# Kernel optimization log

Hardware: AMD Instinct MI355X
Metric: run time of the kernel (lower is better)

## Reference

```python
import jax, jax.numpy as jnp
import numpy as np

NUM_HEADS = 8
CHUNK = 64


def _retention(q, k, v):
    # q, k: (B, H, L, DK); v: (B, H, L, DV). Chunked linear retention with
    # per-head exponential decay gamma_h = 1 - 2^(-5-h) (RetNet convention).
    B, Hn, L, DK = q.shape
    DV = v.shape[-1]
    C = CHUNK
    N = L // C
    dt = q.dtype
    gamma = (1.0 - jnp.exp2(-5.0 - jnp.arange(Hn, dtype=jnp.float32))).astype(dt)  # (H,)
    q = q * (DK ** -0.5)
    idx = jnp.arange(C)
    diff = idx[:, None] - idx[None, :]
    # intra-chunk causal decay mask D[h,i,j] = gamma_h^(i-j) for i>=j else 0
    D = jnp.where(diff >= 0, gamma[:, None, None] ** diff, 0.0).astype(dt)      # (H,C,C)
    decay_q = (gamma[:, None] ** (idx[None, :] + 1)).astype(dt)                 # (H,C)
    decay_k = (gamma[:, None] ** (C - 1 - idx[None, :])).astype(dt)             # (H,C)
    decay_s = (gamma ** C).astype(dt)                                           # (H,)

    def to_chunks(x):
        return jnp.moveaxis(x.reshape(B, Hn, N, C, -1), 2, 0)  # (N,B,H,C,d)

    qs, ks, vs = map(to_chunks, (q, k, v))

    def step(S, x):
        qc, kc, vc = x  # (B,H,C,dk) / (B,H,C,dv)
        attn = jnp.einsum('bhid,bhjd->bhij', qc, kc) * D
        o_intra = jnp.einsum('bhij,bhje->bhie', attn, vc)
        o_inter = jnp.einsum('bhid,bhde->bhie', qc * decay_q[None, :, :, None], S)
        S_new = decay_s[None, :, None, None] * S + jnp.einsum(
            'bhjd,bhje->bhde', kc * decay_k[None, :, :, None], vc)
        return S_new, o_intra + o_inter

    S0 = jnp.zeros((B, Hn, DK, DV), dt)
    _, o = jax.lax.scan(step, S0, (qs, ks, vs))  # (N,B,H,C,DV)
    return jnp.moveaxis(o, 0, 2).reshape(B, Hn, L, DV)


def _xavier(key, fan_in, fan_out, gain=2 ** (-2.5)):
    limit = gain * np.sqrt(6.0 / (fan_in + fan_out))
    return jax.random.uniform(key, (fan_in, fan_out), jnp.float32, -limit, limit)


def setup_inputs() -> dict:
    key = jax.random.key(0)
    k0, k1, k2, k3, k4 = jax.random.split(key, 5)
    B, L, D = 2, 4096, 1024
    return {
        'hidden_states': jax.random.normal(k0, (B, L, D), jnp.float32),
        'rel_pos': jnp.zeros((1,), jnp.float32),  # unused by the module's forward
        'Wq': _xavier(k1, D, D),
        'Wk': _xavier(k2, D, D),
        'Wv': _xavier(k3, D, D),
        'Wo': _xavier(k4, D, D),
    }


def reference(hidden_states, rel_pos, Wq, Wk, Wv, Wo):
    B, L, Dm = hidden_states.shape
    Hd = Dm // NUM_HEADS
    q = (hidden_states @ Wq).reshape(B, L, NUM_HEADS, Hd).transpose(0, 2, 1, 3)
    k = (hidden_states @ Wk).reshape(B, L, NUM_HEADS, Hd).transpose(0, 2, 1, 3)
    v = (hidden_states @ Wv).reshape(B, L, NUM_HEADS, Hd).transpose(0, 2, 1, 3)
    o = _retention(q, k, v)  # (B,H,L,Hd)
    o = o.transpose(0, 2, 1, 3).reshape(B, L, Dm)
    return o @ Wo
```

## Files before the change

### kernel.cpp

```cpp
#include <hip/hip_runtime.h>
#include <hip/hip_bf16.h>

typedef __bf16 bf16;
typedef __bf16 bf16x8 __attribute__((ext_vector_type(8)));
typedef float f32x4 __attribute__((ext_vector_type(4)));

#define MFMA16(a, b, c) __builtin_amdgcn_mfma_f32_16x16x32_bf16((a), (b), (c), 0, 0, 0)


__device__ __forceinline__ void g2l16(const bf16* g, bf16* l) {
  __builtin_amdgcn_global_load_lds(
      (const __attribute__((address_space(1))) void*)g,
      (__attribute__((address_space(3))) void*)l, 16, 0, 0);
}

__global__ __launch_bounds__(256) void cvt_bf16(const float* __restrict__ X,
                                                bf16* __restrict__ Y) {
  const size_t i = ((size_t)blockIdx.x * 256 + threadIdx.x) * 8;
  float4 a = *(const float4*)&X[i];
  float4 b = *(const float4*)&X[i + 4];
  union { bf16 h[8]; uint4 u; } p;
  p.h[0] = (bf16)a.x; p.h[1] = (bf16)a.y; p.h[2] = (bf16)a.z; p.h[3] = (bf16)a.w;
  p.h[4] = (bf16)b.x; p.h[5] = (bf16)b.y; p.h[6] = (bf16)b.z; p.h[7] = (bf16)b.w;
  *(uint4*)&Y[i] = p.u;
}

__global__ __launch_bounds__(256) void transpose_w(
    const float* __restrict__ Wq, const float* __restrict__ Wk,
    const float* __restrict__ Wv, const float* __restrict__ Wo,
    bf16* __restrict__ Wt) {
  __shared__ bf16 t[64 * 72];
  const float* src = (blockIdx.z == 0) ? Wq : (blockIdx.z == 1) ? Wk
                     : (blockIdx.z == 2) ? Wv : Wo;
  bf16* dst = Wt + (size_t)blockIdx.z * 1024 * 1024;
  const int k0 = blockIdx.x * 64, n0 = blockIdx.y * 64;
  const int tid = threadIdx.x;
#pragma unroll
  for (int s = 0; s < 4; ++s) {
    int u = tid + s * 256;
    int r = u >> 4, c4 = (u & 15) * 4;
    float4 f = *(const float4*)&src[(size_t)(k0 + r) * 1024 + n0 + c4];
    t[r * 72 + c4 + 0] = (bf16)f.x;
    t[r * 72 + c4 + 1] = (bf16)f.y;
    t[r * 72 + c4 + 2] = (bf16)f.z;
    t[r * 72 + c4 + 3] = (bf16)f.w;
  }
  __syncthreads();
#pragma unroll
  for (int s = 0; s < 2; ++s) {
    int u = tid + s * 256;
    int r = u >> 3, cc = u & 7;
    union { bf16 h[8]; uint4 u4; } pk;
#pragma unroll
    for (int j = 0; j < 8; ++j) pk.h[j] = t[(cc * 8 + j) * 72 + r];
    *(uint4*)&dst[(size_t)(n0 + r) * 1024 + k0 + cc * 8] = pk.u4;
  }
}

template <typename TC, int QKV>
__global__ __launch_bounds__(256) void gemm_lds(
    const bf16* __restrict__ A, const bf16* __restrict__ Bt,
    TC* __restrict__ C, float alpha) {
  __shared__ bf16 lA[128 * 64];
  __shared__ bf16 lB[128 * 64];
  const int m0 = blockIdx.x * 128, n0 = blockIdx.y * 128;
  if (QKV) {
    Bt += (size_t)blockIdx.z * 1024 * 1024;
    C += (size_t)blockIdx.z * 8192 * 1024;
    if (blockIdx.z != 0) alpha = 1.0f;
  }
  const int tid = threadIdx.x;
  const int w = tid >> 6, lane = tid & 63, lr = lane & 15, quad = lane >> 4;
  const int wm = w >> 1, wn = w & 1;

  const int srow = w * 32 + (lane >> 3);
  const int clog = (lane & 7) ^ ((lane >> 3) & 7);
  const bf16* gA = A + (size_t)(m0 + srow) * 1024 + clog * 8;
  const bf16* gB = Bt + (size_t)(n0 + srow) * 1024 + clog * 8;

  f32x4 acc[4][4] = {};

  for (int it = 0; it < 16; ++it) {
    const int k0 = it * 64;
#pragma unroll
    for (int is = 0; is < 4; ++is) {
      g2l16(gA + (size_t)is * 8 * 1024 + k0, &lA[(w * 32 + is * 8) * 64]);
      g2l16(gB + (size_t)is * 8 * 1024 + k0, &lB[(w * 32 + is * 8) * 64]);
    }
    __syncthreads();
#pragma unroll
    for (int kk = 0; kk < 2; ++kk) {
      bf16x8 af[4], bfv[4];
#pragma unroll
      for (int i = 0; i < 4; ++i) {
        const int m = wm * 64 + i * 16 + lr;
        af[i] = *(bf16x8*)&lA[m * 64 + (((kk * 4 + quad) ^ (lr & 7)) * 8)];
      }
#pragma unroll
      for (int j = 0; j < 4; ++j) {
        const int n = wn * 64 + j * 16 + lr;
        bfv[j] = *(bf16x8*)&lB[n * 64 + (((kk * 4 + quad) ^ (lr & 7)) * 8)];
      }
#pragma unroll
      for (int i = 0; i < 4; ++i)
#pragma unroll
        for (int j = 0; j < 4; ++j)
          acc[i][j] = MFMA16(af[i], bfv[j], acc[i][j]);
    }
    __syncthreads();
  }
#pragma unroll
  for (int i = 0; i < 4; ++i) {
#pragma unroll
    for (int j = 0; j < 4; ++j) {
      const int row = m0 + wm * 64 + i * 16 + quad * 4;
      const int col = n0 + wn * 64 + j * 16 + lr;
#pragma unroll
      for (int r = 0; r < 4; ++r)
        C[(size_t)(row + r) * 1024 + col] = (TC)(acc[i][j][r] * alpha);
    }
  }
}

__global__ __launch_bounds__(256) void chunk_kv(
    const bf16* __restrict__ kb, const bf16* __restrict__ vb,
    bf16* __restrict__ Tb) {
  __shared__ bf16 lK[128 * 72];
  __shared__ bf16 lV[128 * 72];
  const int g = blockIdx.x;
  const int bh = g >> 6, n = g & 63, b = bh >> 3, h = bh & 7;
  const float log2g = log2f(1.0f - exp2f(-5.0f - (float)h));
  const int tid = threadIdx.x;
  const size_t rowbase = (size_t)(b * 4096 + n * 64) * 1024 + h * 128;
  const bf16* kc = kb + rowbase;
  const bf16* vc = vb + rowbase;
#pragma unroll
  for (int s = 0; s < 4; ++s) {
    int u = tid + s * 256;
    int c = u >> 4, d0 = (u & 15) * 8;
    union { uint4 u4; bf16 h8[8]; } kv, vv;
    kv.u4 = *(const uint4*)&kc[(size_t)c * 1024 + d0];
    vv.u4 = *(const uint4*)&vc[(size_t)c * 1024 + d0];
    const float dec = exp2f((float)(63 - c) * log2g);
#pragma unroll
    for (int j = 0; j < 8; ++j) {
      lK[(d0 + j) * 72 + c] = (bf16)((float)kv.h8[j] * dec);
      lV[(d0 + j) * 72 + c] = vv.h8[j];
    }
  }
  __syncthreads();
  const int w = tid >> 6, lane = tid & 63, lr = lane & 15, quad = lane >> 4;
  const int wm = w >> 1, wn = w & 1;
  f32x4 acc[4][4] = {};
#pragma unroll
  for (int kk = 0; kk < 2; ++kk) {
    bf16x8 af[4], bv[4];
#pragma unroll
    for (int i = 0; i < 4; ++i)
      af[i] = *(bf16x8*)&lK[(wm * 64 + i * 16 + lr) * 72 + kk * 32 + quad * 8];
#pragma unroll
    for (int j = 0; j < 4; ++j)
      bv[j] = *(bf16x8*)&lV[(wn * 64 + j * 16 + lr) * 72 + kk * 32 + quad * 8];
#pragma unroll
    for (int i = 0; i < 4; ++i)
#pragma unroll
      for (int j = 0; j < 4; ++j)
        acc[i][j] = MFMA16(af[i], bv[j], acc[i][j]);
  }
  bf16* tchunk = Tb + (size_t)g * 16384;
#pragma unroll
  for (int i = 0; i < 4; ++i) {
#pragma unroll
    for (int j = 0; j < 4; ++j) {
      const int dk = wm * 64 + i * 16 + quad * 4;
      const int dv = wn * 64 + j * 16 + lr;
      union { bf16 h4[4]; uint2 u2; } pk;
#pragma unroll
      for (int r = 0; r < 4; ++r) pk.h4[r] = (bf16)acc[i][j][r];
      *(uint2*)&tchunk[(size_t)dv * 128 + dk] = pk.u2;
    }
  }
}

__global__ __launch_bounds__(256) void scan_state(bf16* __restrict__ Tb) {
  const int blk = blockIdx.x;
  const int bh = blk >> 6, seg = blk & 63, h = bh & 7;
  const float gs = exp2f(64.0f * log2f(1.0f - exp2f(-5.0f - (float)h)));
  const size_t base = (size_t)bh * 64 * 16384 + (size_t)seg * 256 + threadIdx.x;
  float S = 0.0f;
#pragma unroll 8
  for (int n = 0; n < 64; ++n) {
    const size_t a = base + (size_t)n * 16384;
    const float t = (float)Tb[a];
    Tb[a] = (bf16)S;
    S = gs * S + t;
  }
}

__global__ __launch_bounds__(256) void chunk_out(
    const bf16* __restrict__ qb, const bf16* __restrict__ kb,
    const bf16* __restrict__ vb, const bf16* __restrict__ Sp,
    bf16* __restrict__ ob) {
  __shared__ bf16 lQ[64 * 136];
  __shared__ bf16 lK[64 * 136];
  __shared__ bf16 lVt[128 * 72];
  __shared__ bf16 lP[64 * 72];
  const int g = blockIdx.x;
  const int bh = g >> 6, n = g & 63, b = bh >> 3, h = bh & 7;
  const float log2g = log2f(1.0f - exp2f(-5.0f - (float)h));
  const int tid = threadIdx.x;
  const size_t rowbase = (size_t)(b * 4096 + n * 64) * 1024 + h * 128;
  const bf16* qc = qb + rowbase;
  const bf16* kc = kb + rowbase;
  const bf16* vc = vb + rowbase;
#pragma unroll
  for (int s = 0; s < 4; ++s) {
    int u = tid + s * 256;
    int c = u >> 4, d0 = (u & 15) * 8;
    *(uint4*)&lQ[c * 136 + d0] = *(const uint4*)&qc[(size_t)c * 1024 + d0];
    *(uint4*)&lK[c * 136 + d0] = *(const uint4*)&kc[(size_t)c * 1024 + d0];
    union { uint4 u4; bf16 h8[8]; } vv;
    vv.u4 = *(const uint4*)&vc[(size_t)c * 1024 + d0];
#pragma unroll
    for (int j = 0; j < 8; ++j) lVt[(d0 + j) * 72 + c] = vv.h8[j];
  }
  __syncthreads();
  const int w = tid >> 6, lane = tid & 63, lr = lane & 15, quad = lane >> 4;

  f32x4 p[4] = {};
#pragma unroll
  for (int kk = 0; kk < 4; ++kk) {
    bf16x8 bfrag = *(bf16x8*)&lK[(w * 16 + lr) * 136 + kk * 32 + quad * 8];
#pragma unroll
    for (int i = 0; i < 4; ++i) {
      bf16x8 afrag = *(bf16x8*)&lQ[(i * 16 + lr) * 136 + kk * 32 + quad * 8];
      p[i] = MFMA16(afrag, bfrag, p[i]);
    }
  }
#pragma unroll
  for (int i = 0; i < 4; ++i) {
#pragma unroll
    for (int r = 0; r < 4; ++r) {
      const int row = i * 16 + quad * 4 + r;
      const int col = w * 16 + lr;
      const int diff = row - col;
      const float val =
          (diff >= 0) ? p[i][r] * exp2f((float)diff * log2g) : 0.0f;
      lP[row * 72 + col] = (bf16)val;
    }
  }
  __syncthreads();

  f32x4 oacc[4][2] = {};
#pragma unroll
  for (int j = 0; j < 2; ++j) {
    const int dvt = w * 32 + j * 16;
#pragma unroll
    for (int kk = 0; kk < 2; ++kk) {
      bf16x8 bfrag = *(bf16x8*)&lVt[(dvt + lr) * 72 + kk * 32 + quad * 8];
#pragma unroll
      for (int i = 0; i < 4; ++i) {
        bf16x8 afrag = *(bf16x8*)&lP[(i * 16 + lr) * 72 + kk * 32 + quad * 8];
        oacc[i][j] = MFMA16(afrag, bfrag, oacc[i][j]);
      }
    }
  }

  const bf16* sp = Sp + (size_t)g * 16384;
#pragma unroll
  for (int kk = 0; kk < 4; ++kk) {
    bf16x8 aN[4];
#pragma unroll
    for (int i = 0; i < 4; ++i) {
      bf16x8 a0 = *(bf16x8*)&lQ[(i * 16 + lr) * 136 + kk * 32 + quad * 8];
      const float dq = exp2f((float)(i * 16 + lr + 1) * log2g);
#pragma unroll
      for (int e = 0; e < 8; ++e) a0[e] = (bf16)((float)a0[e] * dq);
      aN[i] = a0;
    }
#pragma unroll
    for (int j = 0; j < 2; ++j) {
      bf16x8 bfrag =
          *(const bf16x8*)&sp[(size_t)(w * 32 + j * 16 + lr) * 128 + kk * 32 + quad * 8];
#pragma unroll
      for (int i = 0; i < 4; ++i) oacc[i][j] = MFMA16(aN[i], bfrag, oacc[i][j]);
    }
  }

  bf16* oc = ob + rowbase;
#pragma unroll
  for (int i = 0; i < 4; ++i)
#pragma unroll
    for (int j = 0; j < 2; ++j)
#pragma unroll
      for (int r = 0; r < 4; ++r) {
        const int row = i * 16 + quad * 4 + r;
        const int col = w * 32 + j * 16 + lr;
        oc[(size_t)row * 1024 + col] = (bf16)oacc[i][j][r];
      }
}

extern "C" void kernel_launch(void* const* d_in, const int* in_sizes, int n_in,
                              void* d_out, int out_size, void* d_ws,
                              size_t ws_size, hipStream_t stream) {
  const float* X  = (const float*)d_in[0];
  const float* Wq = (const float*)d_in[2];
  const float* Wk = (const float*)d_in[3];
  const float* Wv = (const float*)d_in[4];
  const float* Wo = (const float*)d_in[5];

  char* ws = (char*)d_ws;
  const size_t SZ_QKV = (size_t)8192 * 1024 * sizeof(bf16);
  bf16* qb = (bf16*)(ws);
  bf16* ob = (bf16*)(ws + 3 * SZ_QKV);
  bf16* Tb = (bf16*)(ws + 4 * SZ_QKV);
  bf16* Wt = (bf16*)(ws + 6 * SZ_QKV);
  bf16* Xb = (bf16*)(ws + 6 * SZ_QKV + (size_t)4 * 1024 * 1024 * sizeof(bf16));
  bf16* kb = qb + (size_t)8192 * 1024;
  bf16* vb = kb + (size_t)8192 * 1024;

  cvt_bf16<<<4096, 256, 0, stream>>>(X, Xb);
  transpose_w<<<dim3(16, 16, 4), 256, 0, stream>>>(Wq, Wk, Wv, Wo, Wt);

  const float qscale = 0.08838834764831845f;
  gemm_lds<bf16, 1><<<dim3(64, 8, 3), 256, 0, stream>>>(Xb, Wt, qb, qscale);

  chunk_kv<<<1024, 256, 0, stream>>>(kb, vb, Tb);
  scan_state<<<1024, 256, 0, stream>>>(Tb);
  chunk_out<<<1024, 256, 0, stream>>>(qb, kb, vb, Tb, ob);

  gemm_lds<float, 0><<<dim3(64, 8), 256, 0, stream>>>(
      ob, Wt + (size_t)3 * 1024 * 1024, (float*)d_out, 1.0f);
}
```

Baseline: 230.9 us.

## Merge prep kernels, swizzle transposed LDS tiles, vectorize state scan, precompute decayed Q

Fuses the input conversion and weight transpose into a single launch. Applies an XOR swizzle to the transposed K/V LDS tiles in chunk_kv and chunk_out to reduce bank conflicts on the strided column writes. Rewrites scan_state so each thread handles 8 contiguous elements with 16-byte loads, using 128 blocks instead of 1024. chunk_out now builds a decay-scaled copy of Q in LDS once, instead of rescaling fragments inside the inter-chunk MMA loop, at the cost of extra shared memory.

```diff
diff --git a/kernel.cpp b/kernel.cpp
--- a/kernel.cpp
+++ b/kernel.cpp
@@ -14,27 +14,32 @@
       (__attribute__((address_space(3))) void*)l, 16, 0, 0);
 }
 
-__global__ __launch_bounds__(256) void cvt_bf16(const float* __restrict__ X,
-                                                bf16* __restrict__ Y) {
-  const size_t i = ((size_t)blockIdx.x * 256 + threadIdx.x) * 8;
-  float4 a = *(const float4*)&X[i];
-  float4 b = *(const float4*)&X[i + 4];
-  union { bf16 h[8]; uint4 u; } p;
-  p.h[0] = (bf16)a.x; p.h[1] = (bf16)a.y; p.h[2] = (bf16)a.z; p.h[3] = (bf16)a.w;
-  p.h[4] = (bf16)b.x; p.h[5] = (bf16)b.y; p.h[6] = (bf16)b.z; p.h[7] = (bf16)b.w;
-  *(uint4*)&Y[i] = p.u;
-}
-
-__global__ __launch_bounds__(256) void transpose_w(
-    const float* __restrict__ Wq, const float* __restrict__ Wk,
-    const float* __restrict__ Wv, const float* __restrict__ Wo,
+__device__ __forceinline__ int swz72(int row, int c) {
+  return row * 72 + (c & 7) + ((((c >> 3) ^ (row >> 3)) & 7) << 3);
+}
+
+__global__ __launch_bounds__(256) void prep(
+    const float* __restrict__ X, const float* __restrict__ Wq,
+    const float* __restrict__ Wk, const float* __restrict__ Wv,
+    const float* __restrict__ Wo, bf16* __restrict__ Xb,
     bf16* __restrict__ Wt) {
   __shared__ bf16 t[64 * 72];
-  const float* src = (blockIdx.z == 0) ? Wq : (blockIdx.z == 1) ? Wk
-                     : (blockIdx.z == 2) ? Wv : Wo;
-  bf16* dst = Wt + (size_t)blockIdx.z * 1024 * 1024;
-  const int k0 = blockIdx.x * 64, n0 = blockIdx.y * 64;
   const int tid = threadIdx.x;
+  if (blockIdx.x < 4096) {
+    const size_t i = ((size_t)blockIdx.x * 256 + tid) * 8;
+    float4 a = *(const float4*)&X[i];
+    float4 b = *(const float4*)&X[i + 4];
+    union { bf16 h[8]; uint4 u; } p;
+    p.h[0] = (bf16)a.x; p.h[1] = (bf16)a.y; p.h[2] = (bf16)a.z; p.h[3] = (bf16)a.w;
+    p.h[4] = (bf16)b.x; p.h[5] = (bf16)b.y; p.h[6] = (bf16)b.z; p.h[7] = (bf16)b.w;
+    *(uint4*)&Xb[i] = p.u;
+    return;
+  }
+  const int bid2 = blockIdx.x - 4096;
+  const int bx = bid2 & 15, by = (bid2 >> 4) & 15, bz = bid2 >> 8;
+  const float* src = (bz == 0) ? Wq : (bz == 1) ? Wk : (bz == 2) ? Wv : Wo;
+  bf16* dst = Wt + (size_t)bz * 1024 * 1024;
+  const int k0 = bx * 64, n0 = by * 64;
 #pragma unroll
   for (int s = 0; s < 4; ++s) {
     int u = tid + s * 256;
@@ -144,8 +149,8 @@
     const float dec = exp2f((float)(63 - c) * log2g);
 #pragma unroll
     for (int j = 0; j < 8; ++j) {
-      lK[(d0 + j) * 72 + c] = (bf16)((float)kv.h8[j] * dec);
-      lV[(d0 + j) * 72 + c] = vv.h8[j];
+      lK[swz72(d0 + j, c)] = (bf16)((float)kv.h8[j] * dec);
+      lV[swz72(d0 + j, c)] = vv.h8[j];
     }
   }
   __syncthreads();
@@ -157,10 +162,10 @@
     bf16x8 af[4], bv[4];
 #pragma unroll
     for (int i = 0; i < 4; ++i)
-      af[i] = *(bf16x8*)&lK[(wm * 64 + i * 16 + lr) * 72 + kk * 32 + quad * 8];
+      af[i] = *(bf16x8*)&lK[swz72(wm * 64 + i * 16 + lr, kk * 32 + quad * 8)];
 #pragma unroll
     for (int j = 0; j < 4; ++j)
-      bv[j] = *(bf16x8*)&lV[(wn * 64 + j * 16 + lr) * 72 + kk * 32 + quad * 8];
+      bv[j] = *(bf16x8*)&lV[swz72(wn * 64 + j * 16 + lr, kk * 32 + quad * 8)];
 #pragma unroll
     for (int i = 0; i < 4; ++i)
 #pragma unroll
@@ -184,16 +189,22 @@
 
 __global__ __launch_bounds__(256) void scan_state(bf16* __restrict__ Tb) {
   const int blk = blockIdx.x;
-  const int bh = blk >> 6, seg = blk & 63, h = bh & 7;
+  const int bh = blk >> 3, seg = blk & 7, h = bh & 7;
   const float gs = exp2f(64.0f * log2f(1.0f - exp2f(-5.0f - (float)h)));
-  const size_t base = (size_t)bh * 64 * 16384 + (size_t)seg * 256 + threadIdx.x;
-  float S = 0.0f;
-#pragma unroll 8
+  const size_t base = (size_t)bh * 64 * 16384 + (size_t)seg * 2048 +
+                      (size_t)threadIdx.x * 8;
+  float S[8] = {0.f, 0.f, 0.f, 0.f, 0.f, 0.f, 0.f, 0.f};
+#pragma unroll 4
   for (int n = 0; n < 64; ++n) {
     const size_t a = base + (size_t)n * 16384;
-    const float t = (float)Tb[a];
-    Tb[a] = (bf16)S;
-    S = gs * S + t;
+    union { uint4 u4; bf16 h8[8]; } in, out;
+    in.u4 = *(const uint4*)&Tb[a];
+#pragma unroll
+    for (int e = 0; e < 8; ++e) {
+      out.h8[e] = (bf16)S[e];
+      S[e] = gs * S[e] + (float)in.h8[e];
+    }
+    *(uint4*)&Tb[a] = out.u4;
   }
 }
 
@@ -202,6 +213,7 @@
     const bf16* __restrict__ vb, const bf16* __restrict__ Sp,
     bf16* __restrict__ ob) {
   __shared__ bf16 lQ[64 * 136];
+  __shared__ bf16 lQd[64 * 136];
   __shared__ bf16 lK[64 * 136];
   __shared__ bf16 lVt[128 * 72];
   __shared__ bf16 lP[64 * 72];
@@ -217,12 +229,17 @@
   for (int s = 0; s < 4; ++s) {
     int u = tid + s * 256;
     int c = u >> 4, d0 = (u & 15) * 8;
-    *(uint4*)&lQ[c * 136 + d0] = *(const uint4*)&qc[(size_t)c * 1024 + d0];
+    union { uint4 u4; bf16 h8[8]; } qv, vv, qd;
+    qv.u4 = *(const uint4*)&qc[(size_t)c * 1024 + d0];
+    *(uint4*)&lQ[c * 136 + d0] = qv.u4;
     *(uint4*)&lK[c * 136 + d0] = *(const uint4*)&kc[(size_t)c * 1024 + d0];
-    union { uint4 u4; bf16 h8[8]; } vv;
+    const float dq = exp2f((float)(c + 1) * log2g);
+#pragma unroll
+    for (int j = 0; j < 8; ++j) qd.h8[j] = (bf16)((float)qv.h8[j] * dq);
+    *(uint4*)&lQd[c * 136 + d0] = qd.u4;
     vv.u4 = *(const uint4*)&vc[(size_t)c * 1024 + d0];
 #pragma unroll
-    for (int j = 0; j < 8; ++j) lVt[(d0 + j) * 72 + c] = vv.h8[j];
+    for (int j = 0; j < 8; ++j) lVt[swz72(d0 + j, c)] = vv.h8[j];
   }
   __syncthreads();
   const int w = tid >> 6, lane = tid & 63, lr = lane & 15, quad = lane >> 4;
@@ -257,7 +274,7 @@
     const int dvt = w * 32 + j * 16;
 #pragma unroll
     for (int kk = 0; kk < 2; ++kk) {
-      bf16x8 bfrag = *(bf16x8*)&lVt[(dvt + lr) * 72 + kk * 32 + quad * 8];
+      bf16x8 bfrag = *(bf16x8*)&lVt[swz72(dvt + lr, kk * 32 + quad * 8)];
 #pragma unroll
       for (int i = 0; i < 4; ++i) {
         bf16x8 afrag = *(bf16x8*)&lP[(i * 16 + lr) * 72 + kk * 32 + quad * 8];
@@ -271,13 +288,8 @@
   for (int kk = 0; kk < 4; ++kk) {
     bf16x8 aN[4];
 #pragma unroll
-    for (int i = 0; i < 4; ++i) {
-      bf16x8 a0 = *(bf16x8*)&lQ[(i * 16 + lr) * 136 + kk * 32 + quad * 8];
-      const float dq = exp2f((float)(i * 16 + lr + 1) * log2g);
-#pragma unroll
-      for (int e = 0; e < 8; ++e) a0[e] = (bf16)((float)a0[e] * dq);
-      aN[i] = a0;
-    }
+    for (int i = 0; i < 4; ++i)
+      aN[i] = *(bf16x8*)&lQd[(i * 16 + lr) * 136 + kk * 32 + quad * 8];
 #pragma unroll
     for (int j = 0; j < 2; ++j) {
       bf16x8 bfrag =
@@ -319,14 +331,13 @@
   bf16* kb = qb + (size_t)8192 * 1024;
   bf16* vb = kb + (size_t)8192 * 1024;
 
-  cvt_bf16<<<4096, 256, 0, stream>>>(X, Xb);
-  transpose_w<<<dim3(16, 16, 4), 256, 0, stream>>>(Wq, Wk, Wv, Wo, Wt);
+  prep<<<5120, 256, 0, stream>>>(X, Wq, Wk, Wv, Wo, Xb, Wt);
 
   const float qscale = 0.08838834764831845f;
   gemm_lds<bf16, 1><<<dim3(64, 8, 3), 256, 0, stream>>>(Xb, Wt, qb, qscale);
 
   chunk_kv<<<1024, 256, 0, stream>>>(kb, vb, Tb);
-  scan_state<<<1024, 256, 0, stream>>>(Tb);
+  scan_state<<<128, 256, 0, stream>>>(Tb);
   chunk_out<<<1024, 256, 0, stream>>>(qb, kb, vb, Tb, ob);
 
   gemm_lds<float, 0><<<dim3(64, 8), 256, 0, stream>>>(
```

New measurement: 229.7 us (median of 2 runs). No clear change (-0.5%).
